# Kernel optimization log

Hardware: AMD Instinct MI355X
Metric: run time of the kernel (lower is better)

The kernel has to match this reference:

```python
import jax, jax.numpy as jnp
import numpy as np

N = 500000   # num instances
C = 64       # num clock regions (8x8 grid)
CHIP_W, CHIP_H = 168.0, 480.0


def setup_inputs() -> dict:
    key = jax.random.key(0)
    k1, k2, k3 = jax.random.split(key, 3)
    # 8x8 grid of clock-region well boxes (xl, yl, xh, yh) tiling the chip
    gx, gy = 8, 8
    cw, ch = CHIP_W / gx, CHIP_H / gy
    ix = np.arange(C) % gx
    iy = np.arange(C) // gx
    well_boxes = jnp.asarray(
        np.stack([ix * cw, iy * ch, (ix + 1) * cw, (iy + 1) * ch], axis=1),
        dtype=jnp.float32)
    # instance centers uniformly over the chip
    inst_pos = jax.random.uniform(k1, (N, 2), dtype=jnp.float32) * jnp.array(
        [CHIP_W, CHIP_H], dtype=jnp.float32)
    # half sizes in [0.25, 0.75) sites (module stores inst_sizes * 0.5)
    half_inst_sizes = jax.random.uniform(k2, (N, 2), dtype=jnp.float32) * 0.5 + 0.25
    inst_areas = 4.0 * half_inst_sizes[:, 0] * half_inst_sizes[:, 1]
    # per-instance candidate CR availability; guarantee >=1 available CR
    avail = jax.random.randint(k3, (N, C), 0, 2) > 0
    avail = avail.at[:, 0].set(True)
    exponents = jnp.full((N,), 2.0, dtype=jnp.float32)
    return {
        'inst_pos': inst_pos,
        'half_inst_sizes': half_inst_sizes,
        'inst_areas': inst_areas,
        'well_boxes': well_boxes,
        'inst_cr_avail_map': avail,
        'exponents': exponents,
    }


def reference(inst_pos, half_inst_sizes, inst_areas, well_boxes,
              inst_cr_avail_map, exponents):
    # Per-instance CR selection + box-overlap well energy.
    x = inst_pos[:, 0:1]           # (N,1)
    y = inst_pos[:, 1:2]
    hx = half_inst_sizes[:, 0:1]
    hy = half_inst_sizes[:, 1:2]
    xl, yl, xh, yh = (well_boxes[:, 0], well_boxes[:, 1],
                      well_boxes[:, 2], well_boxes[:, 3])  # each (C,)
    # protrusion distance of the instance box outside each well box, (N,C)
    dx = jnp.maximum(jnp.maximum(xl - (x - hx), (x + hx) - xh), 0.0)
    dy = jnp.maximum(jnp.maximum(yl - (y - hy), (y + hy) - yh), 0.0)
    dist = dx + dy
    # mask out unavailable clock regions, pick nearest available CR
    dist = jnp.where(inst_cr_avail_map, dist, jnp.inf)
    selected_crs = jnp.argmin(dist, axis=1)  # (N,)
    dx_sel = jnp.take_along_axis(dx, selected_crs[:, None], axis=1)[:, 0]
    dy_sel = jnp.take_along_axis(dy, selected_crs[:, None], axis=1)[:, 0]
    # per-instance exponentiated well energy
    energy = jnp.power(dx_sel, exponents) + jnp.power(dy_sel, exponents)
    return energy
```

## Files before the change

kernel.cpp:

```cpp
#include <hip/hip_runtime.h>
#include <stdint.h>


#define C_WELLS 64

struct TileWork {
    int4   av[4];
    float2 p, h;
    float  e;
};

__device__ __forceinline__ TileWork load_tile(
    const int4* __restrict__ avail4, const float2* __restrict__ inst_pos,
    const float2* __restrict__ half_sizes, const float* __restrict__ exponents,
    int tile, int lane, int N)
{
    TileWork w;
    const int i  = tile * 16 + (lane >> 2);
    const int ii = i < N ? i : N - 1;
    const int4* a = avail4 + ((size_t)ii * 16 + (size_t)(lane & 3) * 4);
    w.av[0] = a[0]; w.av[1] = a[1]; w.av[2] = a[2]; w.av[3] = a[3];
    w.p = inst_pos[ii];
    w.h = half_sizes[ii];
    w.e = exponents[ii];
    return w;
}

__global__ __launch_bounds__(256, 4)
void energy_well_kernel(const float2* __restrict__ inst_pos,
                        const float2* __restrict__ half_sizes,
                        const float*  __restrict__ well_boxes,
                        const int4*   __restrict__ avail4,
                        const float*  __restrict__ exponents,
                        float* __restrict__ out,
                        int N, int nT16)
{
    const int lane = threadIdx.x & 63;
    const int sub  = lane & 3;
    const int waveId = (int)((blockIdx.x * blockDim.x + threadIdx.x) >> 6);
    const int nWaves = (gridDim.x * blockDim.x) >> 6;

    float xlv[8], xhv[8];
    #pragma unroll
    for (int ix = 0; ix < 8; ++ix) {
        xlv[ix] = well_boxes[4 * ix + 0];
        xhv[ix] = well_boxes[4 * ix + 2];
    }
    const float ylA = well_boxes[64 * sub + 1];
    const float yhA = well_boxes[64 * sub + 3];
    const float ylB = well_boxes[64 * sub + 33];
    const float yhB = well_boxes[64 * sub + 35];

    int tile = waveId;
    if (tile >= nT16) return;

    TileWork w = load_tile(avail4, inst_pos, half_sizes, exponents, tile, lane, N);

    while (true) {
        const int nt = tile + nWaves;
        TileWork wn;
        const bool more = nt < nT16;
        if (more)
            wn = load_tile(avail4, inst_pos, half_sizes, exponents, nt, lane, N);

        const float xm = w.p.x - w.h.x, xp_ = w.p.x + w.h.x;
        const float ym = w.p.y - w.h.y, yp_ = w.p.y + w.h.y;

        float dxv[8];
        #pragma unroll
        for (int ix = 0; ix < 8; ++ix)
            dxv[ix] = fmaxf(fmaxf(xlv[ix] - xm, xp_ - xhv[ix]), 0.0f);
        const float dyA = fmaxf(fmaxf(ylA - ym, yp_ - yhA), 0.0f);
        const float dyB = fmaxf(fmaxf(ylB - ym, yp_ - yhB), 0.0f);

        float best = __builtin_inff();
        float bdx = 0.0f, bdy = 0.0f;
        #pragma unroll
        for (int j = 0; j < 4; ++j) {
            const int4 a4 = w.av[j];
            #pragma unroll
            for (int k = 0; k < 4; ++k) {
                const int c2 = 4 * j + k;
                const int av = (k == 0) ? a4.x : (k == 1) ? a4.y
                             : (k == 2) ? a4.z : a4.w;
                const int   ix = c2 & 7;
                const float dy = (c2 < 8) ? dyA : dyB;
                const float dist = dxv[ix] + dy;
                const bool upd = (av != 0) && (dist < best);
                best = upd ? dist    : best;
                bdx  = upd ? dxv[ix] : bdx;
                bdy  = upd ? dy      : bdy;
            }
        }

        const unsigned kb  = __float_as_uint(best);
        unsigned klo = (kb << 2) | (unsigned)sub;
        unsigned khi = kb >> 30;
        const unsigned mylo = klo, myhi = khi;
        #pragma unroll
        for (int off = 1; off <= 2; off <<= 1) {
            const unsigned plo = __shfl_xor(klo, off, 64);
            const unsigned phi = __shfl_xor(khi, off, 64);
            const bool less = (phi < khi) || (phi == khi && plo < klo);
            klo = less ? plo : klo;
            khi = less ? phi : khi;
        }
        const bool winner = (khi == myhi) && (klo == mylo);

        const int i = tile * 16 + (lane >> 2);
        if (winner && i < N) {
            float energy;
            if (w.e == 2.0f) energy = bdx * bdx + bdy * bdy;
            else             energy = powf(bdx, w.e) + powf(bdy, w.e);
            out[i] = energy;
        }

        if (!more) break;
        w = wn;
        tile = nt;
    }
}

extern "C" void kernel_launch(void* const* d_in, const int* in_sizes, int n_in,
                              void* d_out, int out_size, void* d_ws, size_t ws_size,
                              hipStream_t stream)
{
    const float2* inst_pos   = (const float2*)d_in[0];
    const float2* half_sizes = (const float2*)d_in[1];
    const float*  well_boxes = (const float*)d_in[3];
    const int4*   avail4     = (const int4*)d_in[4];
    const float*  exponents  = (const float*)d_in[5];
    float* out = (float*)d_out;

    const int N = in_sizes[5];
    const int nT16 = (N + 15) / 16;

    const int blocks = 1024;
    energy_well_kernel<<<dim3(blocks), dim3(256), 0, stream>>>(
        inst_pos, half_sizes, well_boxes, avail4, exponents, out, N, nT16);
}
```

Before: 199.2 us.

## Use one tile per wave with 64-bit packed argmin keys and DPP reduction

Replaces the persistent grid-stride loop with software prefetch by a full grid in which each wave handles exactly one 16-instance tile. The per-lane argmin is rewritten as a branchless min over 64-bit keys packing the distance bits and the CR index. The cross-lane reduction uses DPP quad permutes instead of ds_bpermute shuffles, and the selected dx/dy are recovered from the index with select trees. Launch bounds are raised to allow more waves per SIMD, relying on occupancy rather than explicit prefetch to hide the memory-bound avail-map reads.

```diff
diff --git a/kernel.cpp b/kernel.cpp
--- a/kernel.cpp
+++ b/kernel.cpp
@@ -4,29 +4,21 @@
 
 #define C_WELLS 64
 
-struct TileWork {
-    int4   av[4];
-    float2 p, h;
-    float  e;
-};
-
-__device__ __forceinline__ TileWork load_tile(
-    const int4* __restrict__ avail4, const float2* __restrict__ inst_pos,
-    const float2* __restrict__ half_sizes, const float* __restrict__ exponents,
-    int tile, int lane, int N)
-{
-    TileWork w;
-    const int i  = tile * 16 + (lane >> 2);
-    const int ii = i < N ? i : N - 1;
-    const int4* a = avail4 + ((size_t)ii * 16 + (size_t)(lane & 3) * 4);
-    w.av[0] = a[0]; w.av[1] = a[1]; w.av[2] = a[2]; w.av[3] = a[3];
-    w.p = inst_pos[ii];
-    w.h = half_sizes[ii];
-    w.e = exponents[ii];
-    return w;
+template <int CTRL>
+__device__ __forceinline__ unsigned long long dpp64(unsigned long long k) {
+    int lo = (int)(unsigned)k;
+    int hi = (int)(unsigned)(k >> 32);
+    lo = __builtin_amdgcn_update_dpp(0, lo, CTRL, 0xF, 0xF, true);
+    hi = __builtin_amdgcn_update_dpp(0, hi, CTRL, 0xF, 0xF, true);
+    return ((unsigned long long)(unsigned)hi << 32) | (unsigned)lo;
 }
 
-__global__ __launch_bounds__(256, 4)
+__device__ __forceinline__ unsigned long long umin64(unsigned long long a,
+                                                     unsigned long long b) {
+    return a < b ? a : b;
+}
+
+__global__ __launch_bounds__(256, 6)
 void energy_well_kernel(const float2* __restrict__ inst_pos,
                         const float2* __restrict__ half_sizes,
                         const float*  __restrict__ well_boxes,
@@ -37,8 +29,17 @@
 {
     const int lane = threadIdx.x & 63;
     const int sub  = lane & 3;
-    const int waveId = (int)((blockIdx.x * blockDim.x + threadIdx.x) >> 6);
-    const int nWaves = (gridDim.x * blockDim.x) >> 6;
+    const int tile = (int)((blockIdx.x * blockDim.x + threadIdx.x) >> 6);
+    if (tile >= nT16) return;
+
+    const int i  = tile * 16 + (lane >> 2);
+    const int ii = i < N ? i : N - 1;
+
+    const int4* a = avail4 + ((size_t)ii * 16 + (size_t)sub * 4);
+    const int4 av0 = a[0], av1 = a[1], av2 = a[2], av3 = a[3];
+    const float2 p = inst_pos[ii];
+    const float2 h = half_sizes[ii];
+    const float  e = exponents[ii];
 
     float xlv[8], xhv[8];
     #pragma unroll
@@ -51,73 +52,58 @@
     const float ylB = well_boxes[64 * sub + 33];
     const float yhB = well_boxes[64 * sub + 35];
 
-    int tile = waveId;
-    if (tile >= nT16) return;
+    const float xm = p.x - h.x, xp_ = p.x + h.x;
+    const float ym = p.y - h.y, yp_ = p.y + h.y;
 
-    TileWork w = load_tile(avail4, inst_pos, half_sizes, exponents, tile, lane, N);
+    float dxv[8];
+    #pragma unroll
+    for (int ix = 0; ix < 8; ++ix)
+        dxv[ix] = fmaxf(fmaxf(xlv[ix] - xm, xp_ - xhv[ix]), 0.0f);
+    const float dyA = fmaxf(fmaxf(ylA - ym, yp_ - yhA), 0.0f);
+    const float dyB = fmaxf(fmaxf(ylB - ym, yp_ - yhB), 0.0f);
 
-    while (true) {
-        const int nt = tile + nWaves;
-        TileWork wn;
-        const bool more = nt < nT16;
-        if (more)
-            wn = load_tile(avail4, inst_pos, half_sizes, exponents, nt, lane, N);
+    const unsigned gbase = (unsigned)(sub << 4);
+    unsigned long long gm[4];
+    #pragma unroll
+    for (int j = 0; j < 4; ++j) {
+        const int4 a4 = (j == 0) ? av0 : (j == 1) ? av1 : (j == 2) ? av2 : av3;
+        unsigned long long acc = ~0ull;
+        #pragma unroll
+        for (int k = 0; k < 4; ++k) {
+            const int c2 = 4 * j + k;
+            const int avw = (k == 0) ? a4.x : (k == 1) ? a4.y
+                          : (k == 2) ? a4.z : a4.w;
+            const float dy   = (c2 < 8) ? dyA : dyB;
+            const float dist = dxv[c2 & 7] + dy;
+            unsigned long long key =
+                (((unsigned long long)__float_as_uint(dist)) << 6)
+                | (unsigned long long)(gbase + (unsigned)c2);
+            key = avw ? key : ~0ull;
+            acc = umin64(acc, key);
+        }
+        gm[j] = acc;
+    }
+    unsigned long long kmin = umin64(umin64(gm[0], gm[1]), umin64(gm[2], gm[3]));
 
-        const float xm = w.p.x - w.h.x, xp_ = w.p.x + w.h.x;
-        const float ym = w.p.y - w.h.y, yp_ = w.p.y + w.h.y;
+    kmin = umin64(kmin, dpp64<0xB1>(kmin));
+    kmin = umin64(kmin, dpp64<0x4E>(kmin));
 
-        float dxv[8];
-        #pragma unroll
-        for (int ix = 0; ix < 8; ++ix)
-            dxv[ix] = fmaxf(fmaxf(xlv[ix] - xm, xp_ - xhv[ix]), 0.0f);
-        const float dyA = fmaxf(fmaxf(ylA - ym, yp_ - yhA), 0.0f);
-        const float dyB = fmaxf(fmaxf(ylB - ym, yp_ - yhB), 0.0f);
+    const int g = (int)(kmin & 63);
+    const int s = g & 7;
+    float a0 = (s & 1) ? dxv[1] : dxv[0];
+    float a1 = (s & 1) ? dxv[3] : dxv[2];
+    float a2 = (s & 1) ? dxv[5] : dxv[4];
+    float a3 = (s & 1) ? dxv[7] : dxv[6];
+    float b0 = (s & 2) ? a1 : a0;
+    float b1 = (s & 2) ? a3 : a2;
+    const float dxs = (s & 4) ? b1 : b0;
+    const float dys = (g & 8) ? dyB : dyA;
 
-        float best = __builtin_inff();
-        float bdx = 0.0f, bdy = 0.0f;
-        #pragma unroll
-        for (int j = 0; j < 4; ++j) {
-            const int4 a4 = w.av[j];
-            #pragma unroll
-            for (int k = 0; k < 4; ++k) {
-                const int c2 = 4 * j + k;
-                const int av = (k == 0) ? a4.x : (k == 1) ? a4.y
-                             : (k == 2) ? a4.z : a4.w;
-                const int   ix = c2 & 7;
-                const float dy = (c2 < 8) ? dyA : dyB;
-                const float dist = dxv[ix] + dy;
-                const bool upd = (av != 0) && (dist < best);
-                best = upd ? dist    : best;
-                bdx  = upd ? dxv[ix] : bdx;
-                bdy  = upd ? dy      : bdy;
-            }
-        }
-
-        const unsigned kb  = __float_as_uint(best);
-        unsigned klo = (kb << 2) | (unsigned)sub;
-        unsigned khi = kb >> 30;
-        const unsigned mylo = klo, myhi = khi;
-        #pragma unroll
-        for (int off = 1; off <= 2; off <<= 1) {
-            const unsigned plo = __shfl_xor(klo, off, 64);
-            const unsigned phi = __shfl_xor(khi, off, 64);
-            const bool less = (phi < khi) || (phi == khi && plo < klo);
-            klo = less ? plo : klo;
-            khi = less ? phi : khi;
-        }
-        const bool winner = (khi == myhi) && (klo == mylo);
-
-        const int i = tile * 16 + (lane >> 2);
-        if (winner && i < N) {
-            float energy;
-            if (w.e == 2.0f) energy = bdx * bdx + bdy * bdy;
-            else             energy = powf(bdx, w.e) + powf(bdy, w.e);
-            out[i] = energy;
-        }
-
-        if (!more) break;
-        w = wn;
-        tile = nt;
+    if (((g >> 4) == sub) && (i < N)) {
+        float energy;
+        if (e == 2.0f) energy = dxs * dxs + dys * dys;
+        else           energy = powf(dxs, e) + powf(dys, e);
+        out[i] = energy;
     }
 }
 
@@ -134,8 +120,8 @@
 
     const int N = in_sizes[5];
     const int nT16 = (N + 15) / 16;
+    const int blocks = (nT16 + 3) / 4;
 
-    const int blocks = 1024;
     energy_well_kernel<<<dim3(blocks), dim3(256), 0, stream>>>(
         inst_pos, half_sizes, well_boxes, avail4, exponents, out, N, nT16);
 }
```

New measurement: 196.3 us. About the same (-1.4%).
